# Optimization experiments

Hardware: AMD Instinct MI355X
Metric: run time of the kernel (lower is better)

## Reference

```python
import jax, jax.numpy as jnp
import numpy as np

H_DIM = 256
N_HEADS = 8
HEAD_DIM = H_DIM // N_HEADS
B, N = 2, 2048
LN_EPS = 1e-5


def setup_inputs() -> dict:
    key = jax.random.key(0)
    ks = jax.random.split(key, 20)
    s = 1.0 / np.sqrt(H_DIM)
    inp = {
        'hidden': jax.random.normal(ks[0], (B, N, H_DIM), jnp.float32),
        'adjacency': jax.random.uniform(ks[1], (B, N, N), jnp.float32),
        'positions': jax.random.uniform(ks[2], (B, N, 2), jnp.float32),
        # linear weights stored as (in, out): y = x @ W + b
        'wq': jax.random.normal(ks[3], (H_DIM, H_DIM), jnp.float32) * s,
        'bq': jnp.zeros((H_DIM,), jnp.float32),
        'wk': jax.random.normal(ks[4], (H_DIM, H_DIM), jnp.float32) * s,
        'bk': jnp.zeros((H_DIM,), jnp.float32),
        'wv': jax.random.normal(ks[5], (H_DIM, H_DIM), jnp.float32) * s,
        'bv': jnp.zeros((H_DIM,), jnp.float32),
        'wo': jax.random.normal(ks[6], (H_DIM, H_DIM), jnp.float32) * s,
        'bo': jnp.zeros((H_DIM,), jnp.float32),
        'g1': jnp.ones((H_DIM,), jnp.float32),
        'b1': jnp.zeros((H_DIM,), jnp.float32),
        'g2': jnp.ones((H_DIM,), jnp.float32),
        'b2': jnp.zeros((H_DIM,), jnp.float32),
        'w_ff1': jax.random.normal(ks[7], (H_DIM, 4 * H_DIM), jnp.float32) * s,
        'b_ff1': jnp.zeros((4 * H_DIM,), jnp.float32),
        'w_ff2': jax.random.normal(ks[8], (4 * H_DIM, H_DIM), jnp.float32) * (1.0 / np.sqrt(4 * H_DIM)),
        'b_ff2': jnp.zeros((H_DIM,), jnp.float32),
    }
    return inp


def _layernorm(x, g, b):
    mu = jnp.mean(x, axis=-1, keepdims=True)
    var = jnp.var(x, axis=-1, keepdims=True)
    return (x - mu) * jax.lax.rsqrt(var + LN_EPS) * g + b


def reference(hidden, adjacency, positions, wq, bq, wk, bk, wv, bv, wo, bo,
              g1, b1, g2, b2, w_ff1, b_ff1, w_ff2, b_ff2):
    b_, n_, _ = hidden.shape
    normalized = _layernorm(hidden, g1, b1)
    # project and split heads: [B, H, N, Dh]
    def heads(x):
        return x.reshape(b_, n_, N_HEADS, HEAD_DIM).transpose(0, 2, 1, 3)
    q = heads(normalized @ wq + bq)
    k = heads(normalized @ wk + bk)
    v = heads(normalized @ wv + bv)
    logits = jnp.einsum('bhnd,bhmd->bhnm', q, k) / np.sqrt(HEAD_DIM)
    cond = adjacency[:, None, :, :]  # mode == 'connectivity'
    logits = logits + (2.0 * cond - 1.0)
    weights = jax.nn.softmax(logits, axis=-1)
    weights = weights * (0.25 + 0.75 * cond)
    weights = weights / jnp.maximum(weights.sum(axis=-1, keepdims=True), 1e-6)
    attended = jnp.einsum('bhnm,bhmd->bhnd', weights, v)
    attended = attended.transpose(0, 2, 1, 3).reshape(b_, n_, H_DIM)
    hidden = hidden + attended @ wo + bo
    h2 = _layernorm(hidden, g2, b2)
    ff = jax.nn.gelu(h2 @ w_ff1 + b_ff1, approximate=False) @ w_ff2 + b_ff2
    return hidden + ff
```

## Files before the change

kernel.cpp:

```cpp
#include <hip/hip_runtime.h>
#include <math.h>

#define BB 2
#define NN 2048
#define HD 256
#define NH 8
#define DH 32
#define NTOK (BB*NN)
#define QKVLD 768
#define NSPLIT 4

typedef _Float16 h8 __attribute__((ext_vector_type(8)));
typedef _Float16 h4 __attribute__((ext_vector_type(4)));
typedef float fx4 __attribute__((ext_vector_type(4)));

#define LOG2E 1.4426950408889634f
#define SQ_LOG2 0.25503486f
#define C1A (2.0f * LOG2E)
#define C0A (-(LOG2E + 6.0f))

__device__ __forceinline__ void ln_row(const float* __restrict__ x,
    const float* __restrict__ g, const float* __restrict__ bta,
    _Float16* __restrict__ yh, int row, int lane)
{
  const float* xr = x + (size_t)row * HD + lane * 4;
  float4 v = *(const float4*)xr;
  float s = v.x + v.y + v.z + v.w;
  #pragma unroll
  for (int off = 32; off > 0; off >>= 1) s += __shfl_xor(s, off);
  float mu = s * (1.0f / HD);
  float dx0 = v.x - mu, dx1 = v.y - mu, dx2 = v.z - mu, dx3 = v.w - mu;
  float ss = dx0*dx0 + dx1*dx1 + dx2*dx2 + dx3*dx3;
  #pragma unroll
  for (int off = 32; off > 0; off >>= 1) ss += __shfl_xor(ss, off);
  float rinv = rsqrtf(ss * (1.0f / HD) + 1e-5f);
  float4 gv = *(const float4*)(g   + lane * 4);
  float4 bv = *(const float4*)(bta + lane * 4);
  h4 hh;
  hh[0] = (_Float16)(dx0 * rinv * gv.x + bv.x);
  hh[1] = (_Float16)(dx1 * rinv * gv.y + bv.y);
  hh[2] = (_Float16)(dx2 * rinv * gv.z + bv.z);
  hh[3] = (_Float16)(dx3 * rinv * gv.w + bv.w);
  *(h4*)(yh + (size_t)row * HD + lane * 4) = hh;
}

__global__ __launch_bounds__(256) void ln_kernel(const float* __restrict__ x,
    const float* __restrict__ g, const float* __restrict__ bta,
    _Float16* __restrict__ yh)
{
  ln_row(x, g, bta, yh, blockIdx.x * 4 + (threadIdx.x >> 6), threadIdx.x & 63);
}

__device__ __forceinline__ void do_transpose(const float* __restrict__ W,
    _Float16* __restrict__ Wh, int Nw, int rowoff, int ldout, float scale,
    int bx, int by, float (*tile)[33])
{
  int k0 = by * 32, n0 = bx * 32;
  int c = threadIdx.x & 31, r = threadIdx.x >> 5;
  #pragma unroll
  for (int i = 0; i < 4; i++)
    tile[r + i * 8][c] = W[(size_t)(k0 + r + i * 8) * Nw + n0 + c];
  __syncthreads();
  #pragma unroll
  for (int i = 0; i < 4; i++) {
    int n = r + i * 8;
    Wh[(size_t)(rowoff + n0 + n) * ldout + k0 + c] = (_Float16)(tile[c][n] * scale);
  }
}

__global__ __launch_bounds__(256) void prep_kernel(
    const float* wq, const float* wk, const float* wv, const float* wo,
    const float* wf1, const float* wf2,
    const float* bq, const float* bk, const float* bv,
    const float* hidden, const float* g1, const float* b1,
    _Float16* WtQKVh, _Float16* WtOh, _Float16* WtF1h, _Float16* WtF2h,
    float* biasqkv, _Float16* norm1h)
{
  __shared__ float tile[32][33];
  int bid = blockIdx.x;
  if (bid < 64)        do_transpose(wq,  WtQKVh,  256,   0,  256, SQ_LOG2, bid & 7, bid >> 3, tile);
  else if (bid < 128)  do_transpose(wk,  WtQKVh,  256, 256,  256, 1.0f, (bid-64) & 7, (bid-64) >> 3, tile);
  else if (bid < 192)  do_transpose(wv,  WtQKVh,  256, 512,  256, 1.0f, (bid-128) & 7, (bid-128) >> 3, tile);
  else if (bid < 256)  do_transpose(wo,  WtOh,    256,   0,  256, 1.0f, (bid-192) & 7, (bid-192) >> 3, tile);
  else if (bid < 512)  do_transpose(wf1, WtF1h,  1024,   0,  256, 1.0f, (bid-256) & 31, (bid-256) >> 5, tile);
  else if (bid < 768)  do_transpose(wf2, WtF2h,   256,   0, 1024, 1.0f, (bid-512) & 7, (bid-512) >> 3, tile);
  else if (bid == 768) {
    #pragma unroll
    for (int j = 0; j < 3; j++) {
      int t = j * 256 + threadIdx.x;
      biasqkv[t] = (t < 256) ? bq[t] * SQ_LOG2 : (t < 512) ? bk[t - 256] : bv[t - 512];
    }
  } else {
    ln_row(hidden, g1, b1, norm1h, (bid - 769) * 4 + (threadIdx.x >> 6), threadIdx.x & 63);
  }
}

template<int KK, int NT, int NX, int ACT, int RES, int OM>
__global__ __launch_bounds__(256) void gemm16_kernel(
    const _Float16* __restrict__ Ah, const _Float16* __restrict__ Wh,
    const float* __restrict__ bias, const float* __restrict__ resid,
    float* __restrict__ Cf, _Float16* __restrict__ Ch,
    _Float16* __restrict__ vtb, int N)
{
  const int lin = blockIdx.x;
  const int qch = gridDim.x >> 3;
  const int wg = (lin & 7) * qch + (lin >> 3);
  const int bx = wg % NX, by = wg / NX;
  const int n0 = bx * (NT * 16);
  const int m0 = by * 64;
  const int t = threadIdx.x, w = t >> 6, l = t & 63;
  const int ml = l & 15, g = l >> 4;
  const int mrow = m0 + w * 16 + ml;

  const _Float16* aph = Ah + (size_t)mrow * KK + g * 8;
  const _Float16* whp[NT];
  #pragma unroll
  for (int nt = 0; nt < NT; nt++)
    whp[nt] = Wh + (size_t)(n0 + nt * 16 + ml) * KK + g * 8;

  fx4 acc[NT];
  #pragma unroll
  for (int nt = 0; nt < NT; nt++) acc[nt] = (fx4){0.f, 0.f, 0.f, 0.f};

  #pragma unroll 4
  for (int k0 = 0; k0 < KK; k0 += 32) {
    h8 ah = *(const h8*)(aph + k0);
    #pragma unroll
    for (int nt = 0; nt < NT; nt++) {
      h8 wh = *(const h8*)(whp[nt] + k0);
      acc[nt] = __builtin_amdgcn_mfma_f32_16x16x32_f16(ah, wh, acc[nt], 0, 0, 0);
    }
  }

  #pragma unroll
  for (int nt = 0; nt < NT; nt++) {
    int n = n0 + nt * 16 + ml;
    float bv = bias[n];
    #pragma unroll
    for (int i = 0; i < 4; i++) {
      int m = m0 + w * 16 + 4 * g + i;
      float vv = acc[nt][i] + bv;
      if (ACT == 1) vv = 0.5f * vv * (1.0f + erff(vv * 0.70710678118654752f));
      if (RES)      vv += resid[(size_t)m * N + n];
      if (OM == 0) {
        Cf[(size_t)m * N + n] = vv;
      } else if (OM == 1) {
        Ch[(size_t)m * N + n] = (_Float16)vv;
      } else {
        if (n < 512) Ch[(size_t)m * QKVLD + n] = (_Float16)vv;
        else {
          int dim = n - 512, kv = m & (NN - 1), bb = m >> 11;
          int kvp = (kv & ~31) | ((kv & 15) << 1) | ((kv >> 4) & 1);
          vtb[((size_t)(bb * HD + dim)) * NN + kvp] = (_Float16)vv;
        }
      }
    }
  }
}

__global__ __launch_bounds__(256) void attn_mfma_kernel(
    const _Float16* __restrict__ qkv16, const _Float16* __restrict__ vtb,
    const float* __restrict__ adj,
    _Float16* __restrict__ Opart, float* __restrict__ Spart)
{
  __shared__ _Float16 Ksh[2][64][40];
  __shared__ _Float16 Vp[2][32][72];
  __shared__ _Float16 AdjL[2][64][68];

  const int z = blockIdx.z;
  const int b = z >> 2, quarter = z & 3;
  const int h = blockIdx.y;
  const int q0 = blockIdx.x * 64;
  const int t = threadIdx.x;
  const int w = t >> 6, l = t & 63;
  const int m = l & 15, g = l >> 4;
  const int kvbase = quarter * (NN / NSPLIT);
  const int NTILES = NN / NSPLIT / 64;

  const int qrow = q0 + w * 16 + m;
  h8 qh = *(const h8*)(qkv16 + ((size_t)(b * NN + qrow)) * QKVLD + h * DH + g * 8);

  fx4 ot0 = {0.f, 0.f, 0.f, 0.f};
  fx4 ot1 = {0.f, 0.f, 0.f, 0.f};
  float S = 0.0f;

  const int arow0 = t >> 4, acol = (t & 15) * 4;
  const float* adjbase = adj + ((size_t)(b * NN + q0)) * NN + kvbase;

  const int krow = t >> 2, kd0 = (t & 3) * 8;
  const int vdim = t >> 3, vkc = (t & 7) * 8;
  const _Float16* kbase = qkv16 + ((size_t)(b * NN + kvbase + krow)) * QKVLD + 256 + h * DH + kd0;
  const _Float16* vbase = vtb + ((size_t)(b * HD + h * DH + vdim)) * NN + kvbase + vkc;

  h8 kreg = *(const h8*)kbase;
  h8 vreg = *(const h8*)vbase;

  {
    float4 ar[4];
    #pragma unroll
    for (int j = 0; j < 4; j++)
      ar[j] = *(const float4*)(adjbase + (size_t)(j * 16 + arow0) * NN + acol);
    #pragma unroll
    for (int j = 0; j < 4; j++) {
      h4 hh;
      hh[0] = (_Float16)ar[j].x; hh[1] = (_Float16)ar[j].y;
      hh[2] = (_Float16)ar[j].z; hh[3] = (_Float16)ar[j].w;
      *(h4*)&AdjL[0][j * 16 + arow0][acol] = hh;
    }
  }
  *(h8*)&Ksh[0][krow][kd0] = kreg;
  *(h8*)&Vp[0][vdim][vkc]  = vreg;
  kreg = *(const h8*)(kbase + (size_t)64 * QKVLD);
  vreg = *(const h8*)(vbase + 64);
  __syncthreads();

  for (int tt = 0; tt < NTILES; ++tt) {
    const int cur = tt & 1;

    float4 ar[4];
    if (tt + 1 < NTILES) {
      #pragma unroll
      for (int j = 0; j < 4; j++)
        ar[j] = *(const float4*)(adjbase + (size_t)(j * 16 + arow0) * NN
                                 + (tt + 1) * 64 + acol);
    }

    h8 kh0 = *(const h8*)&Ksh[cur][     m][g * 8];
    h8 kh1 = *(const h8*)&Ksh[cur][16 + m][g * 8];
    h8 kh2 = *(const h8*)&Ksh[cur][32 + m][g * 8];
    h8 kh3 = *(const h8*)&Ksh[cur][48 + m][g * 8];
    fx4 z4 = {0.f, 0.f, 0.f, 0.f};
    fx4 st[4];
    st[0] = __builtin_amdgcn_mfma_f32_16x16x32_f16(kh0, qh, z4, 0, 0, 0);
    st[1] = __builtin_amdgcn_mfma_f32_16x16x32_f16(kh1, qh, z4, 0, 0, 0);
    st[2] = __builtin_amdgcn_mfma_f32_16x16x32_f16(kh2, qh, z4, 0, 0, 0);
    st[3] = __builtin_amdgcn_mfma_f32_16x16x32_f16(kh3, qh, z4, 0, 0, 0);

    float pv[16];
    #pragma unroll
    for (int p = 0; p < 4; p++) {
      h4 ah4 = *(const h4*)&AdjL[cur][w * 16 + m][p * 16 + g * 4];
      #pragma unroll
      for (int i = 0; i < 4; i++) {
        float a = (float)ah4[i];
        float e = __builtin_amdgcn_exp2f(st[p][i] + C1A * a + C0A);
        float pp = (0.25f + 0.75f * a) * e;
        pv[p * 4 + i] = pp;
        S += pp;
      }
    }
    h8 ph0, ph1;
    #pragma unroll
    for (int q2 = 0; q2 < 4; q2++) {
      ph0[2*q2]     = (_Float16)pv[q2];
      ph0[2*q2 + 1] = (_Float16)pv[4 + q2];
      ph1[2*q2]     = (_Float16)pv[8 + q2];
      ph1[2*q2 + 1] = (_Float16)pv[12 + q2];
    }

    h8 v00 = *(const h8*)&Vp[cur][m][g * 8];
    h8 v01 = *(const h8*)&Vp[cur][m][32 + g * 8];
    h8 v10 = *(const h8*)&Vp[cur][16 + m][g * 8];
    h8 v11 = *(const h8*)&Vp[cur][16 + m][32 + g * 8];
    ot0 = __builtin_amdgcn_mfma_f32_16x16x32_f16(v00, ph0, ot0, 0, 0, 0);
    ot0 = __builtin_amdgcn_mfma_f32_16x16x32_f16(v01, ph1, ot0, 0, 0, 0);
    ot1 = __builtin_amdgcn_mfma_f32_16x16x32_f16(v10, ph0, ot1, 0, 0, 0);
    ot1 = __builtin_amdgcn_mfma_f32_16x16x32_f16(v11, ph1, ot1, 0, 0, 0);

    if (tt + 1 < NTILES) {
      #pragma unroll
      for (int j = 0; j < 4; j++) {
        h4 hh;
        hh[0] = (_Float16)ar[j].x; hh[1] = (_Float16)ar[j].y;
        hh[2] = (_Float16)ar[j].z; hh[3] = (_Float16)ar[j].w;
        *(h4*)&AdjL[cur ^ 1][j * 16 + arow0][acol] = hh;
      }
      *(h8*)&Ksh[cur ^ 1][krow][kd0] = kreg;
      *(h8*)&Vp[cur ^ 1][vdim][vkc]  = vreg;
      if (tt + 2 < NTILES) {
        kreg = *(const h8*)(kbase + (size_t)((tt + 2) * 64) * QKVLD);
        vreg = *(const h8*)(vbase + (tt + 2) * 64);
      }
    }
    __syncthreads();
  }

  S += __shfl_xor(S, 16);
  S += __shfl_xor(S, 32);

  float is = 1.0f / S;
  size_t prow = ((size_t)(z * NH + h)) * NN + qrow;
  _Float16* po = Opart + prow * 32;
  h4 o0h, o1h;
  #pragma unroll
  for (int j = 0; j < 4; j++) {
    o0h[j] = (_Float16)(ot0[j] * is);
    o1h[j] = (_Float16)(ot1[j] * is);
  }
  *(h4*)(po + 4 * g)      = o0h;
  *(h4*)(po + 16 + 4 * g) = o1h;
  if (g == 0) Spart[prow] = S;
}

__global__ __launch_bounds__(256) void attn_combine_kernel(
    const _Float16* __restrict__ Opart, const float* __restrict__ Spart,
    _Float16* __restrict__ atth)
{
  int idx = blockIdx.x * 256 + threadIdx.x;
  int dg  = idx & 7;
  int rowid = idx >> 3;
  int qrow = rowid & (NN - 1);
  int bh = rowid >> 11;
  int b = bh >> 3, h = bh & 7;
  size_t p[NSPLIT];
  float sz[NSPLIT];
  float den = 0.f;
  #pragma unroll
  for (int zq = 0; zq < NSPLIT; zq++) {
    p[zq] = ((size_t)((b * NSPLIT + zq) * NH + h)) * NN + qrow;
    sz[zq] = Spart[p[zq]];
    den += sz[zq];
  }
  float is = 1.0f / den;
  float ov[4] = {0.f, 0.f, 0.f, 0.f};
  #pragma unroll
  for (int zq = 0; zq < NSPLIT; zq++) {
    h4 o = *(const h4*)(Opart + p[zq] * 32 + dg * 4);
    float wzz = sz[zq] * is;
    #pragma unroll
    for (int j = 0; j < 4; j++) ov[j] += wzz * (float)o[j];
  }
  h4 hh;
  #pragma unroll
  for (int j = 0; j < 4; j++) hh[j] = (_Float16)ov[j];
  *(h4*)(atth + ((size_t)(b * NN + qrow)) * HD + h * DH + dg * 4) = hh;
}

extern "C" void kernel_launch(void* const* d_in, const int* in_sizes, int n_in,
                              void* d_out, int out_size, void* d_ws, size_t ws_size,
                              hipStream_t stream)
{
  const float* hidden    = (const float*)d_in[0];
  const float* adjacency = (const float*)d_in[1];
  const float* wq  = (const float*)d_in[3];
  const float* bq  = (const float*)d_in[4];
  const float* wk  = (const float*)d_in[5];
  const float* bk  = (const float*)d_in[6];
  const float* wv  = (const float*)d_in[7];
  const float* bv  = (const float*)d_in[8];
  const float* wo  = (const float*)d_in[9];
  const float* bo  = (const float*)d_in[10];
  const float* g1  = (const float*)d_in[11];
  const float* b1  = (const float*)d_in[12];
  const float* g2  = (const float*)d_in[13];
  const float* b2  = (const float*)d_in[14];
  const float* wf1 = (const float*)d_in[15];
  const float* bf1 = (const float*)d_in[16];
  const float* wf2 = (const float*)d_in[17];
  const float* bf2 = (const float*)d_in[18];
  float* out = (float*)d_out;

  char* base = (char*)d_ws;
  const size_t MB = 1024 * 1024;
  _Float16* norm1h = (_Float16*)(base);
  _Float16* qkv16  = (_Float16*)(base + 2*MB);
  _Float16* vtb    = (_Float16*)(base + 8*MB);
  _Float16* atth   = (_Float16*)(base + 10*MB);
  float*    hid2   = (float*)(base + 12*MB);
  _Float16* Opart = (_Float16*)(base + 16*MB);
  _Float16* ffah  = (_Float16*)(base + 16*MB);
  float* Spart = (float*)(base + 25*MB);
  _Float16* wtb = (_Float16*)(base + 26*MB);
  _Float16* WtQKVh = wtb; wtb += 768 * 256;
  _Float16* WtOh   = wtb; wtb += 256 * 256;
  _Float16* WtF1h  = wtb; wtb += 1024 * 256;
  _Float16* WtF2h  = wtb; wtb += 256 * 1024;
  float* biasqkv = (float*)(base + 28*MB);

  prep_kernel<<<1793, 256, 0, stream>>>(wq, wk, wv, wo, wf1, wf2, bq, bk, bv,
      hidden, g1, b1, WtQKVh, WtOh, WtF1h, WtF2h, biasqkv, norm1h);

  gemm16_kernel<256, 4, 12, 0, 0, 2><<<768, 256, 0, stream>>>(
      norm1h, WtQKVh, biasqkv, nullptr, nullptr, qkv16, vtb, QKVLD);

  attn_mfma_kernel<<<dim3(NN / 64, NH, BB * NSPLIT), 256, 0, stream>>>(
      qkv16, vtb, adjacency, Opart, Spart);
  attn_combine_kernel<<<(BB * NH * NN * 8) / 256, 256, 0, stream>>>(
      Opart, Spart, atth);

  gemm16_kernel<256, 2, 8, 0, 1, 0><<<512, 256, 0, stream>>>(
      atth, WtOh, bo, hidden, hid2, nullptr, nullptr, 256);

  ln_kernel<<<NTOK / 4, 256, 0, stream>>>(hid2, g2, b2, norm1h);

  gemm16_kernel<256, 4, 16, 1, 0, 1><<<1024, 256, 0, stream>>>(
      norm1h, WtF1h, bf1, nullptr, nullptr, ffah, nullptr, 1024);

  gemm16_kernel<1024, 2, 8, 0, 1, 0><<<512, 256, 0, stream>>>(
      ffah, WtF2h, bf2, hid2, out, nullptr, nullptr, 256);
}
```

Before: 120.5 us.

## Fuse split-KV attention combine into output projection GEMM and halve KV splits

Removes the separate attention combine kernel and the atth intermediate buffer. A new MFMA kernel merges the two split-KV partial outputs per head on the fly, weighting them by their partial sums, then multiplies by Wo and adds bias and residual. NSPLIT drops from 4 to 2, so each attention block walks twice as many KV tiles and the grid is half as large. This saves a launch and global traffic for Opart and atth, but reduces attention parallelism and the new GEMM does no LDS reuse of Wo.

```diff
diff --git a/kernel.cpp b/kernel.cpp
--- a/kernel.cpp
+++ b/kernel.cpp
@@ -8,7 +8,9 @@
 #define DH 32
 #define NTOK (BB*NN)
 #define QKVLD 768
-#define NSPLIT 4
+#define NSPLIT 2
+#define KVPB (NN/NSPLIT)
+#define NTILES (KVPB/64)
 
 typedef _Float16 h8 __attribute__((ext_vector_type(8)));
 typedef _Float16 h4 __attribute__((ext_vector_type(4)));
@@ -158,6 +160,56 @@
   }
 }
 
+__global__ __launch_bounds__(256) void wo_fused_kernel(
+    const _Float16* __restrict__ Opart, const float* __restrict__ Spart,
+    const _Float16* __restrict__ Wh, const float* __restrict__ bias,
+    const float* __restrict__ resid, float* __restrict__ Cf)
+{
+  const int lin = blockIdx.x;
+  const int qch = gridDim.x >> 3;
+  const int wg = (lin & 7) * qch + (lin >> 3);
+  const int bx = wg & 7, by = wg >> 3;
+  const int n0 = bx * 32;
+  const int m0 = by * 64;
+  const int t = threadIdx.x, w = t >> 6, l = t & 63;
+  const int ml = l & 15, g = l >> 4;
+  const int mrow = m0 + w * 16 + ml;
+  const int bb = mrow >> 11, qrow = mrow & (NN - 1);
+
+  const _Float16* whp0 = Wh + (size_t)(n0 + ml) * HD + g * 8;
+  const _Float16* whp1 = Wh + (size_t)(n0 + 16 + ml) * HD + g * 8;
+
+  fx4 acc0 = {0.f, 0.f, 0.f, 0.f};
+  fx4 acc1 = {0.f, 0.f, 0.f, 0.f};
+
+  #pragma unroll
+  for (int h = 0; h < NH; h++) {
+    size_t p0 = ((size_t)((bb * 2 + 0) * NH + h)) * NN + qrow;
+    size_t p1 = ((size_t)((bb * 2 + 1) * NH + h)) * NN + qrow;
+    float s0 = Spart[p0], s1 = Spart[p1];
+    float den = 1.0f / (s0 + s1);
+    float w0 = s0 * den, w1 = s1 * den;
+    h8 o0 = *(const h8*)(Opart + p0 * 32 + g * 8);
+    h8 o1 = *(const h8*)(Opart + p1 * 32 + g * 8);
+    h8 ah;
+    #pragma unroll
+    for (int j = 0; j < 8; j++)
+      ah[j] = (_Float16)(w0 * (float)o0[j] + w1 * (float)o1[j]);
+    h8 wh0 = *(const h8*)(whp0 + h * 32);
+    h8 wh1 = *(const h8*)(whp1 + h * 32);
+    acc0 = __builtin_amdgcn_mfma_f32_16x16x32_f16(ah, wh0, acc0, 0, 0, 0);
+    acc1 = __builtin_amdgcn_mfma_f32_16x16x32_f16(ah, wh1, acc1, 0, 0, 0);
+  }
+
+  #pragma unroll
+  for (int i = 0; i < 4; i++) {
+    int m = m0 + w * 16 + 4 * g + i;
+    int na = n0 + ml, nb = n0 + 16 + ml;
+    Cf[(size_t)m * HD + na] = acc0[i] + bias[na] + resid[(size_t)m * HD + na];
+    Cf[(size_t)m * HD + nb] = acc1[i] + bias[nb] + resid[(size_t)m * HD + nb];
+  }
+}
+
 __global__ __launch_bounds__(256) void attn_mfma_kernel(
     const _Float16* __restrict__ qkv16, const _Float16* __restrict__ vtb,
     const float* __restrict__ adj,
@@ -168,14 +220,13 @@
   __shared__ _Float16 AdjL[2][64][68];
 
   const int z = blockIdx.z;
-  const int b = z >> 2, quarter = z & 3;
+  const int b = z >> 1, half = z & 1;
   const int h = blockIdx.y;
   const int q0 = blockIdx.x * 64;
   const int t = threadIdx.x;
   const int w = t >> 6, l = t & 63;
   const int m = l & 15, g = l >> 4;
-  const int kvbase = quarter * (NN / NSPLIT);
-  const int NTILES = NN / NSPLIT / 64;
+  const int kvbase = half * KVPB;
 
   const int qrow = q0 + w * 16 + m;
   h8 qh = *(const h8*)(qkv16 + ((size_t)(b * NN + qrow)) * QKVLD + h * DH + g * 8);
@@ -300,40 +351,6 @@
   *(h4*)(po + 4 * g)      = o0h;
   *(h4*)(po + 16 + 4 * g) = o1h;
   if (g == 0) Spart[prow] = S;
-}
-
-__global__ __launch_bounds__(256) void attn_combine_kernel(
-    const _Float16* __restrict__ Opart, const float* __restrict__ Spart,
-    _Float16* __restrict__ atth)
-{
-  int idx = blockIdx.x * 256 + threadIdx.x;
-  int dg  = idx & 7;
-  int rowid = idx >> 3;
-  int qrow = rowid & (NN - 1);
-  int bh = rowid >> 11;
-  int b = bh >> 3, h = bh & 7;
-  size_t p[NSPLIT];
-  float sz[NSPLIT];
-  float den = 0.f;
-  #pragma unroll
-  for (int zq = 0; zq < NSPLIT; zq++) {
-    p[zq] = ((size_t)((b * NSPLIT + zq) * NH + h)) * NN + qrow;
-    sz[zq] = Spart[p[zq]];
-    den += sz[zq];
-  }
-  float is = 1.0f / den;
-  float ov[4] = {0.f, 0.f, 0.f, 0.f};
-  #pragma unroll
-  for (int zq = 0; zq < NSPLIT; zq++) {
-    h4 o = *(const h4*)(Opart + p[zq] * 32 + dg * 4);
-    float wzz = sz[zq] * is;
-    #pragma unroll
-    for (int j = 0; j < 4; j++) ov[j] += wzz * (float)o[j];
-  }
-  h4 hh;
-  #pragma unroll
-  for (int j = 0; j < 4; j++) hh[j] = (_Float16)ov[j];
-  *(h4*)(atth + ((size_t)(b * NN + qrow)) * HD + h * DH + dg * 4) = hh;
 }
 
 extern "C" void kernel_launch(void* const* d_in, const int* in_sizes, int n_in,
@@ -365,7 +382,6 @@
   _Float16* norm1h = (_Float16*)(base);
   _Float16* qkv16  = (_Float16*)(base + 2*MB);
   _Float16* vtb    = (_Float16*)(base + 8*MB);
-  _Float16* atth   = (_Float16*)(base + 10*MB);
   float*    hid2   = (float*)(base + 12*MB);
   _Float16* Opart = (_Float16*)(base + 16*MB);
   _Float16* ffah  = (_Float16*)(base + 16*MB);
@@ -385,11 +401,9 @@
 
   attn_mfma_kernel<<<dim3(NN / 64, NH, BB * NSPLIT), 256, 0, stream>>>(
       qkv16, vtb, adjacency, Opart, Spart);
-  attn_combine_kernel<<<(BB * NH * NN * 8) / 256, 256, 0, stream>>>(
-      Opart, Spart, atth);
-
-  gemm16_kernel<256, 2, 8, 0, 1, 0><<<512, 256, 0, stream>>>(
-      atth, WtOh, bo, hidden, hid2, nullptr, nullptr, 256);
+
+  wo_fused_kernel<<<512, 256, 0, stream>>>(
+      Opart, Spart, WtOh, bo, hidden, hid2);
 
   ln_kernel<<<NTOK / 4, 256, 0, stream>>>(hid2, g2, b2, norm1h);
 
```

New measurement: 121.4 us. About the same (+0.8%).
